# Performance work log

Hardware: AMD Instinct MI355X
Metric: run time of the kernel (lower is better)

Reference implementation:

```python
import jax, jax.numpy as jnp
import numpy as np

BETA = 0.25
B, D, H, W = 32, 256, 32, 32
K = 1024


def setup_inputs() -> dict:
    key = jax.random.key(0)
    k1, k2 = jax.random.split(key)
    inputs = jax.random.normal(k1, (B, D, H, W), dtype=jnp.float32)
    # torch init: uniform(-1/K, 1/K)
    codebook = jax.random.uniform(k2, (K, D), dtype=jnp.float32,
                                  minval=-1.0 / K, maxval=1.0 / K)
    return {"inputs": inputs, "codebook": codebook}


def reference(inputs, codebook):
    b, d, h, w = inputs.shape
    # (B, C, H, W) -> (B*H*W, D)
    x = inputs.transpose(0, 2, 3, 1).reshape(b * h * w, d)
    # Squared Euclidean distances; argmin is identical to cdist argmin.
    x2 = jnp.sum(x * x, axis=1, keepdims=True)            # (N, 1)
    c2 = jnp.sum(codebook * codebook, axis=1)             # (K,)
    d2 = x2 - 2.0 * (x @ codebook.T) + c2[None, :]        # (N, K)
    idx = jnp.argmin(d2, axis=1)                          # (N,)
    q = codebook[idx].reshape(b, h, w, d).transpose(0, 3, 1, 2)  # (B, D, H, W)

    q_loss = jnp.mean((q - jax.lax.stop_gradient(inputs)) ** 2)
    e_loss = jnp.mean((jax.lax.stop_gradient(q) - inputs) ** 2)
    vq_loss = q_loss + BETA * e_loss

    # straight-through estimator
    quantized = inputs + jax.lax.stop_gradient(q - inputs)
    return quantized, q_loss, e_loss, vq_loss, idx.reshape(b, h, w)
```

## Files before the change

kernel.cpp:

```cpp
#include <hip/hip_runtime.h>
#include <cstdint>

typedef float floatx4 __attribute__((ext_vector_type(4)));
typedef _Float16 half8 __attribute__((ext_vector_type(8)));
typedef _Float16 half4v __attribute__((ext_vector_type(4)));

#define D_DIM 256
#define HW 1024
#define K_CODES 1024
#define NPIX 32768
#define NELEM 8388608

#define OFF_QLOSS 8388608
#define OFF_ELOSS 8388609
#define OFF_VQ    8388610
#define OFF_IDX   8388611

#define WS_IDX     0
#define WS_C2      131072
#define WS_CNT     135168
#define WS_PART    135232
#define WS_FLAGPX  143424
#define WS_FLAGTOP 176192
#define WS_CBS     438336
#define FLAG_CAP   8192

#define MARGIN 2.5e-4f

__device__ __forceinline__ float np_pairwise_sq_256(const float* __restrict__ a, int stride) {
    float half[2];
#pragma unroll
    for (int h = 0; h < 2; ++h) {
        const float* p = a + (size_t)(h * 128) * stride;
        float r[8];
#pragma unroll
        for (int j = 0; j < 8; ++j) { float t = p[(size_t)j * stride]; r[j] = __fmul_rn(t, t); }
        for (int i = 8; i < 128; i += 8)
#pragma unroll
            for (int j = 0; j < 8; ++j) {
                float t = p[(size_t)(i + j) * stride];
                r[j] = __fadd_rn(r[j], __fmul_rn(t, t));
            }
        half[h] = __fadd_rn(__fadd_rn(__fadd_rn(r[0], r[1]), __fadd_rn(r[2], r[3])),
                            __fadd_rn(__fadd_rn(r[4], r[5]), __fadd_rn(r[6], r[7])));
    }
    return __fadd_rn(half[0], half[1]);
}

__global__ __launch_bounds__(256) void prep_kernel(const float* __restrict__ cb,
                                                   _Float16* __restrict__ cbs,
                                                   float* __restrict__ c2,
                                                   int* __restrict__ cnt) {
    int b = blockIdx.x;
    if (b < 256) {
        int idx = b * 256 + threadIdx.x;
        int c = idx >> 6;
        int d = (idx & 63) * 4;
        int s = d >> 5, q = (d >> 3) & 3, j0 = d & 7;
        int half = c >> 9, ch = (c >> 4) & 31, l15 = c & 15;
        int lane = q * 16 + l15;
        size_t o = ((((size_t)(half * 32 + ch) * 8 + s) * 64 + lane) * 8 + j0);
        floatx4 v = *(const floatx4*)(cb + (size_t)c * D_DIM + d);
        half4v h;
#pragma unroll
        for (int j = 0; j < 4; ++j) h[j] = (_Float16)(v[j] * 1024.0f);
        *(half4v*)(cbs + o) = h;
    } else {
        if (b == 256 && threadIdx.x == 0) *cnt = 0;
        int k = (b - 256) * 256 + threadIdx.x;
        c2[k] = np_pairwise_sq_256(cb + (size_t)k * D_DIM, 1);
    }
}

__device__ __forceinline__ void ins4v(float v, int k, float* S, int* I) {
    if (v < S[3]) {
        S[3] = v; I[3] = k;
#pragma unroll
        for (int j = 3; j > 0; --j) {
            if (S[j] < S[j - 1]) {
                float ts = S[j]; S[j] = S[j - 1]; S[j - 1] = ts;
                int   ti = I[j]; I[j] = I[j - 1]; I[j - 1] = ti;
            }
        }
    }
}

__global__ __launch_bounds__(256, 2) void gemm_swz(
        const float* __restrict__ x, const _Float16* __restrict__ cbs,
        const float* __restrict__ c2, float* __restrict__ out_idx,
        int* __restrict__ idxbuf, int* __restrict__ cnt,
        int* __restrict__ flagPx, floatx4* __restrict__ flagTop) {
    __shared__ float scr[4][32 * 65];

    const int t = threadIdx.x;
    const int w = t >> 6;
    const int l = t & 63;
    const int l15 = l & 15;
    const int q = l >> 4;
    const int pxg = w >> 1;
    const int half = w & 1;
    const int px0 = blockIdx.x * 64;
    const int bimg = px0 >> 10;
    const int hwb = (px0 & 1023) + pxg * 32;
    const float* xb = x + (size_t)bimg * (D_DIM * HW);

    half8 A[2][8];
#pragma unroll
    for (int r = 0; r < 2; ++r) {
        float tmp[64];
#pragma unroll
        for (int s = 0; s < 8; ++s)
#pragma unroll
            for (int j = 0; j < 8; ++j)
                tmp[s * 8 + j] = xb[(size_t)(s * 32 + q * 8 + j) * HW + hwb + r * 16 + l15];
#pragma unroll
        for (int s = 0; s < 8; ++s) {
            half8 h;
#pragma unroll
            for (int j = 0; j < 8; ++j) h[j] = (_Float16)tmp[s * 8 + j];
            A[r][s] = h;
        }
    }

    const _Float16* base = cbs + (size_t)half * 131072;
    half8 B[2][8];
#pragma unroll
    for (int s = 0; s < 8; ++s)
        B[0][s] = *(const half8*)(base + (size_t)s * 512 + l * 8);
    float c2cur = c2[half * 512 + l15];

    float m1[2][4], m2[2][4]; int i1[2][4], i2[2][4];
#pragma unroll
    for (int r = 0; r < 2; ++r)
#pragma unroll
        for (int a = 0; a < 4; ++a) {
            m1[r][a] = INFINITY; m2[r][a] = INFINITY; i1[r][a] = 0; i2[r][a] = 0;
        }

#pragma unroll 4
    for (int ch = 0; ch < 32; ++ch) {
        const int cur = ch & 1, nxt = cur ^ 1;
        float c2n = 0.f;
        if (ch < 31) {
            const _Float16* nb = base + (size_t)(ch + 1) * 4096;
#pragma unroll
            for (int s = 0; s < 8; ++s)
                B[nxt][s] = *(const half8*)(nb + (size_t)s * 512 + l * 8);
            c2n = c2[half * 512 + (ch + 1) * 16 + l15];
        }
        floatx4 ac[2][2];
#pragma unroll
        for (int r = 0; r < 2; ++r)
#pragma unroll
            for (int h = 0; h < 2; ++h) ac[r][h] = floatx4{0.f, 0.f, 0.f, 0.f};
#pragma unroll
        for (int s = 0; s < 4; ++s) {
            ac[0][0] = __builtin_amdgcn_mfma_f32_16x16x32_f16(A[0][s],     B[cur][s],     ac[0][0], 0, 0, 0);
            ac[1][0] = __builtin_amdgcn_mfma_f32_16x16x32_f16(A[1][s],     B[cur][s],     ac[1][0], 0, 0, 0);
            ac[0][1] = __builtin_amdgcn_mfma_f32_16x16x32_f16(A[0][s + 4], B[cur][s + 4], ac[0][1], 0, 0, 0);
            ac[1][1] = __builtin_amdgcn_mfma_f32_16x16x32_f16(A[1][s + 4], B[cur][s + 4], ac[1][1], 0, 0, 0);
        }
        const int code = half * 512 + ch * 16 + l15;
#pragma unroll
        for (int r = 0; r < 2; ++r)
#pragma unroll
            for (int a = 0; a < 4; ++a) {
                float dot = ac[r][0][a] + ac[r][1][a];
                float s = fmaf(-0.001953125f, dot, c2cur);
                if (s < m1[r][a]) { m2[r][a] = m1[r][a]; i2[r][a] = i1[r][a]; m1[r][a] = s; i1[r][a] = code; }
                else if (s < m2[r][a]) { m2[r][a] = s; i2[r][a] = code; }
            }
        c2cur = c2n;
    }

    const int part = half * 16 + l15;
#pragma unroll
    for (int r = 0; r < 2; ++r)
#pragma unroll
        for (int a = 0; a < 4; ++a) {
            int px = pxg * 32 + r * 16 + q * 4 + a;
            int o = part * 65 + px;
            scr[0][o] = m1[r][a];
            scr[1][o] = __int_as_float(i1[r][a]);
            scr[2][o] = m2[r][a];
            scr[3][o] = __int_as_float(i2[r][a]);
        }
    __syncthreads();
    if (t < 64) {
        float S[4] = {INFINITY, INFINITY, INFINITY, INFINITY};
        int   I[4] = {0x7fffffff, 0x7fffffff, 0x7fffffff, 0x7fffffff};
        for (int p = 0; p < 32; ++p) {
            int o = p * 65 + t;
            ins4v(scr[0][o], __float_as_int(scr[1][o]), S, I);
            ins4v(scr[2][o], __float_as_int(scr[3][o]), S, I);
        }
        int P = px0 + t;
        idxbuf[P] = I[0];
        out_idx[P] = (float)I[0];
        if (S[1] - S[0] <= MARGIN) {
            int pos = atomicAdd(cnt, 1);
            if (pos < FLAG_CAP) {
                flagPx[pos] = P;
                flagTop[2 * pos]     = floatx4{S[0], (float)I[0], S[1], (float)I[1]};
                flagTop[2 * pos + 1] = floatx4{S[2], (float)I[2], S[3], (float)I[3]};
            }
        }
    }
}

__global__ __launch_bounds__(256) void rescore_wave(
        const float* __restrict__ x, const float* __restrict__ cb,
        const float* __restrict__ c2, const int* __restrict__ cnt,
        const int* __restrict__ flagPx, const floatx4* __restrict__ flagTop,
        float* __restrict__ out_idx, int* __restrict__ idxbuf) {
    const int wglobal = blockIdx.x * 4 + (threadIdx.x >> 6);
    const int l = threadIdx.x & 63;
    int n = *cnt; if (n > FLAG_CAP) n = FLAG_CAP;
    for (int i = wglobal; i < n; i += 1024) {
        int P = flagPx[i];
        floatx4 ta = flagTop[2 * i], tb = flagTop[2 * i + 1];
        float s1 = ta[0];
        float cs[4] = {ta[0], ta[2], tb[0], tb[2]};
        int   ck[4] = {(int)ta[1], (int)ta[3], (int)tb[1], (int)tb[3]};
        int nc = 1;
        while (nc < 4 && cs[nc] - s1 <= MARGIN) ++nc;

        const float* xcol = x + (size_t)(P >> 10) * D_DIM * HW + (P & 1023);

        float rj = 0.f;
        if (l < 16) {
            int h = l >> 3, j = l & 7;
            const float* p = xcol + (size_t)(h * 128) * HW;
            float v0 = p[(size_t)j * HW];
            rj = __fmul_rn(v0, v0);
            for (int ii = 1; ii < 16; ++ii) {
                float v = p[(size_t)(ii * 8 + j) * HW];
                rj = __fadd_rn(rj, __fmul_rn(v, v));
            }
        }
        float r0 = __shfl(rj, 0), r1 = __shfl(rj, 1), r2 = __shfl(rj, 2), r3 = __shfl(rj, 3);
        float r4 = __shfl(rj, 4), r5 = __shfl(rj, 5), r6 = __shfl(rj, 6), r7 = __shfl(rj, 7);
        float h0 = __fadd_rn(__fadd_rn(__fadd_rn(r0, r1), __fadd_rn(r2, r3)),
                             __fadd_rn(__fadd_rn(r4, r5), __fadd_rn(r6, r7)));
        r0 = __shfl(rj, 8); r1 = __shfl(rj, 9); r2 = __shfl(rj, 10); r3 = __shfl(rj, 11);
        r4 = __shfl(rj, 12); r5 = __shfl(rj, 13); r6 = __shfl(rj, 14); r7 = __shfl(rj, 15);
        float h1 = __fadd_rn(__fadd_rn(__fadd_rn(r0, r1), __fadd_rn(r2, r3)),
                             __fadd_rn(__fadd_rn(r4, r5), __fadd_rn(r6, r7)));
        float x2 = __fadd_rn(h0, h1);

        float xv[4];
#pragma unroll
        for (int u = 0; u < 4; ++u) xv[u] = xcol[(size_t)(l + u * 64) * HW];
        double accd[4] = {0.0, 0.0, 0.0, 0.0};
        for (int jc = 0; jc < nc; ++jc) {
            const float* cr = cb + (size_t)ck[jc] * D_DIM;
            double a = 0.0;
#pragma unroll
            for (int u = 0; u < 4; ++u) a += (double)xv[u] * (double)cr[l + u * 64];
#pragma unroll
            for (int off = 32; off > 0; off >>= 1) a += __shfl_down(a, off);
            accd[jc] = a;
        }
        if (l == 0) {
            float bd = INFINITY; int bi = 0x7fffffff;
            for (int jc = 0; jc < nc; ++jc) {
                float mm = (float)accd[jc];
                float t1 = __fsub_rn(x2, __fmul_rn(2.0f, mm));
                float Dq = __fadd_rn(t1, c2[ck[jc]]);
                if (Dq < bd || (Dq == bd && ck[jc] < bi)) { bd = Dq; bi = ck[jc]; }
            }
            idxbuf[P] = bi;
            out_idx[P] = (float)bi;
        }
    }
}

__global__ __launch_bounds__(256) void quantize_loss_kernel(
        const float* __restrict__ x, const float* __restrict__ cb,
        const int* __restrict__ idxbuf, float* __restrict__ out_q,
        double* __restrict__ partials) {
    const int t = threadIdx.x;
    const int pxl = t & 31;
    const int dg = t >> 5;
    const int P = blockIdx.x * 32 + pxl;
    const int bimg = P >> 10, hw = P & 1023;
    const float* xb = x + (size_t)bimg * D_DIM * HW + hw;
    float* qb = out_q + (size_t)bimg * D_DIM * HW + hw;
    const floatx4* crow = (const floatx4*)(cb + (size_t)idxbuf[P] * D_DIM) + dg * 8;
    float lsum = 0.f;
#pragma unroll
    for (int i = 0; i < 8; ++i) {
        floatx4 cv = crow[i];
        int dbase = dg * 32 + i * 4;
#pragma unroll
        for (int j = 0; j < 4; ++j) {
            size_t off = (size_t)(dbase + j) * HW;
            float xv = xb[off];
            qb[off] = cv[j];
            float df = cv[j] - xv;
            lsum = fmaf(df, df, lsum);
        }
    }
    double ds = (double)lsum;
#pragma unroll
    for (int off = 32; off > 0; off >>= 1) ds += __shfl_down(ds, off);
    __shared__ double sred[4];
    if ((t & 63) == 0) sred[t >> 6] = ds;
    __syncthreads();
    if (t == 0) partials[blockIdx.x] = sred[0] + sred[1] + sred[2] + sred[3];
}

__global__ __launch_bounds__(64) void finalize_loss(const double* __restrict__ partials,
                                                    float* __restrict__ out) {
    double s = 0.0;
    for (int i = threadIdx.x; i < 1024; i += 64) s += partials[i];
#pragma unroll
    for (int off = 32; off > 0; off >>= 1) s += __shfl_down(s, off);
    if (threadIdx.x == 0) {
        double m = s / (double)NELEM;
        out[OFF_QLOSS] = (float)m;
        out[OFF_ELOSS] = (float)m;
        out[OFF_VQ]    = (float)(1.25 * m);
    }
}

extern "C" void kernel_launch(void* const* d_in, const int* in_sizes, int n_in,
                              void* d_out, int out_size, void* d_ws, size_t ws_size,
                              hipStream_t stream) {
    const float* x  = (const float*)d_in[0];
    const float* cb = (const float*)d_in[1];
    float* out = (float*)d_out;
    char* ws = (char*)d_ws;

    int*      idxbuf  = (int*)(ws + WS_IDX);
    float*    c2      = (float*)(ws + WS_C2);
    int*      cnt     = (int*)(ws + WS_CNT);
    double*   partials= (double*)(ws + WS_PART);
    int*      flagPx  = (int*)(ws + WS_FLAGPX);
    floatx4*  flagTop = (floatx4*)(ws + WS_FLAGTOP);
    _Float16* cbs     = (_Float16*)(ws + WS_CBS);

    prep_kernel<<<260, 256, 0, stream>>>(cb, cbs, c2, cnt);
    gemm_swz<<<NPIX / 64, 256, 0, stream>>>(x, cbs, c2, out + OFF_IDX, idxbuf,
                                            cnt, flagPx, flagTop);
    rescore_wave<<<256, 256, 0, stream>>>(x, cb, c2, cnt, flagPx, flagTop,
                                          out + OFF_IDX, idxbuf);
    quantize_loss_kernel<<<NPIX / 32, 256, 0, stream>>>(x, cb, idxbuf, out, partials);
    finalize_loss<<<1, 64, 0, stream>>>(partials, out);
}
```

Baseline: 152.9 us.

## Fuse quantize and loss into GEMM epilogue, patch rescored pixels with delta loss

The quantize/loss pass is folded into the end of the distance GEMM kernel. Each block gathers its chosen codebook rows, writes the quantized output and sums the squared error right away, so the separate quantize kernel and the index buffer are no longer needed. The rescore kernel now rewrites the output columns only for pixels whose index changed, and adds the loss difference to a double accumulator with an atomic. The B-fragment prefetch is also deepened from one chunk ahead to two, at the cost of more registers, which could hurt occupancy at the two-blocks-per-CU bound.

```diff
diff --git a/kernel.cpp b/kernel.cpp
--- a/kernel.cpp
+++ b/kernel.cpp
@@ -16,13 +16,13 @@
 #define OFF_VQ    8388610
 #define OFF_IDX   8388611
 
-#define WS_IDX     0
-#define WS_C2      131072
-#define WS_CNT     135168
-#define WS_PART    135232
-#define WS_FLAGPX  143424
-#define WS_FLAGTOP 176192
-#define WS_CBS     438336
+#define WS_C2      0
+#define WS_CNT     4096
+#define WS_LFIX    4160
+#define WS_PART    4224
+#define WS_FLAGPX  8320
+#define WS_FLAGTOP 41088
+#define WS_CBS     303232
 #define FLAG_CAP   8192
 
 #define MARGIN 2.5e-4f
@@ -50,7 +50,8 @@
 __global__ __launch_bounds__(256) void prep_kernel(const float* __restrict__ cb,
                                                    _Float16* __restrict__ cbs,
                                                    float* __restrict__ c2,
-                                                   int* __restrict__ cnt) {
+                                                   int* __restrict__ cnt,
+                                                   double* __restrict__ lossFix) {
     int b = blockIdx.x;
     if (b < 256) {
         int idx = b * 256 + threadIdx.x;
@@ -67,6 +68,7 @@
         *(half4v*)(cbs + o) = h;
     } else {
         if (b == 256 && threadIdx.x == 0) *cnt = 0;
+        if (b == 257 && threadIdx.x == 0) *lossFix = 0.0;
         int k = (b - 256) * 256 + threadIdx.x;
         c2[k] = np_pairwise_sq_256(cb + (size_t)k * D_DIM, 1);
     }
@@ -86,11 +88,14 @@
 }
 
 __global__ __launch_bounds__(256, 2) void gemm_swz(
-        const float* __restrict__ x, const _Float16* __restrict__ cbs,
-        const float* __restrict__ c2, float* __restrict__ out_idx,
-        int* __restrict__ idxbuf, int* __restrict__ cnt,
+        const float* __restrict__ x, const float* __restrict__ cb,
+        const _Float16* __restrict__ cbs, const float* __restrict__ c2,
+        float* __restrict__ out_idx, float* __restrict__ out_q,
+        double* __restrict__ partials, int* __restrict__ cnt,
         int* __restrict__ flagPx, floatx4* __restrict__ flagTop) {
     __shared__ float scr[4][32 * 65];
+    __shared__ int sidx[64];
+    __shared__ double sredd[4];
 
     const int t = threadIdx.x;
     const int w = t >> 6;
@@ -123,11 +128,15 @@
     }
 
     const _Float16* base = cbs + (size_t)half * 131072;
-    half8 B[2][8];
-#pragma unroll
-    for (int s = 0; s < 8; ++s)
+    half8 B[4][8];
+#pragma unroll
+    for (int s = 0; s < 8; ++s) {
         B[0][s] = *(const half8*)(base + (size_t)s * 512 + l * 8);
-    float c2cur = c2[half * 512 + l15];
+        B[1][s] = *(const half8*)(base + 4096 + (size_t)s * 512 + l * 8);
+    }
+    float c2b[4];
+    c2b[0] = c2[half * 512 + l15];
+    c2b[1] = c2[half * 512 + 16 + l15];
 
     float m1[2][4], m2[2][4]; int i1[2][4], i2[2][4];
 #pragma unroll
@@ -139,14 +148,14 @@
 
 #pragma unroll 4
     for (int ch = 0; ch < 32; ++ch) {
-        const int cur = ch & 1, nxt = cur ^ 1;
-        float c2n = 0.f;
-        if (ch < 31) {
-            const _Float16* nb = base + (size_t)(ch + 1) * 4096;
+        const int cur = ch & 3;
+        if (ch < 30) {
+            const int pf = (ch + 2) & 3;
+            const _Float16* nb = base + (size_t)(ch + 2) * 4096;
 #pragma unroll
             for (int s = 0; s < 8; ++s)
-                B[nxt][s] = *(const half8*)(nb + (size_t)s * 512 + l * 8);
-            c2n = c2[half * 512 + (ch + 1) * 16 + l15];
+                B[pf][s] = *(const half8*)(nb + (size_t)s * 512 + l * 8);
+            c2b[pf] = c2[half * 512 + (ch + 2) * 16 + l15];
         }
         floatx4 ac[2][2];
 #pragma unroll
@@ -161,6 +170,7 @@
             ac[1][1] = __builtin_amdgcn_mfma_f32_16x16x32_f16(A[1][s + 4], B[cur][s + 4], ac[1][1], 0, 0, 0);
         }
         const int code = half * 512 + ch * 16 + l15;
+        const float c2cur = c2b[cur];
 #pragma unroll
         for (int r = 0; r < 2; ++r)
 #pragma unroll
@@ -170,7 +180,6 @@
                 if (s < m1[r][a]) { m2[r][a] = m1[r][a]; i2[r][a] = i1[r][a]; m1[r][a] = s; i1[r][a] = code; }
                 else if (s < m2[r][a]) { m2[r][a] = s; i2[r][a] = code; }
             }
-        c2cur = c2n;
     }
 
     const int part = half * 16 + l15;
@@ -195,7 +204,7 @@
             ins4v(scr[2][o], __float_as_int(scr[3][o]), S, I);
         }
         int P = px0 + t;
-        idxbuf[P] = I[0];
+        sidx[t] = I[0];
         out_idx[P] = (float)I[0];
         if (S[1] - S[0] <= MARGIN) {
             int pos = atomicAdd(cnt, 1);
@@ -206,13 +215,45 @@
             }
         }
     }
-}
-
-__global__ __launch_bounds__(256) void rescore_wave(
+    __syncthreads();
+
+    {
+        const int dq = t >> 6;
+        const int pxl = t & 63;
+        const int myidx = sidx[pxl];
+        const int hwofs = (px0 & 1023) + pxl;
+        const float* xcol = x + (size_t)bimg * (D_DIM * HW) + hwofs;
+        float* qcol = out_q + (size_t)bimg * (D_DIM * HW) + hwofs;
+        const floatx4* crow = (const floatx4*)(cb + (size_t)myidx * D_DIM) + dq * 16;
+        float lsum = 0.f;
+#pragma unroll
+        for (int i = 0; i < 16; ++i) {
+            floatx4 cv = crow[i];
+            int dbase = dq * 64 + i * 4;
+#pragma unroll
+            for (int j = 0; j < 4; ++j) {
+                size_t off = (size_t)(dbase + j) * HW;
+                float xv = xcol[off];
+                qcol[off] = cv[j];
+                float df = cv[j] - xv;
+                lsum = fmaf(df, df, lsum);
+            }
+        }
+        double ds = (double)lsum;
+#pragma unroll
+        for (int off = 32; off > 0; off >>= 1) ds += __shfl_down(ds, off);
+        if (l == 0) sredd[w] = ds;
+    }
+    __syncthreads();
+    if (t == 0) partials[blockIdx.x] = sredd[0] + sredd[1] + sredd[2] + sredd[3];
+}
+
+__global__ __launch_bounds__(256) void rescore_fix(
         const float* __restrict__ x, const float* __restrict__ cb,
         const float* __restrict__ c2, const int* __restrict__ cnt,
         const int* __restrict__ flagPx, const floatx4* __restrict__ flagTop,
-        float* __restrict__ out_idx, int* __restrict__ idxbuf) {
+        float* __restrict__ out_idx, float* __restrict__ out_q,
+        double* __restrict__ lossFix) {
     const int wglobal = blockIdx.x * 4 + (threadIdx.x >> 6);
     const int l = threadIdx.x & 63;
     int n = *cnt; if (n > FLAG_CAP) n = FLAG_CAP;
@@ -225,7 +266,8 @@
         int nc = 1;
         while (nc < 4 && cs[nc] - s1 <= MARGIN) ++nc;
 
-        const float* xcol = x + (size_t)(P >> 10) * D_DIM * HW + (P & 1023);
+        const size_t colbase = (size_t)(P >> 10) * (D_DIM * HW) + (P & 1023);
+        const float* xcol = x + colbase;
 
         float rj = 0.f;
         if (l < 16) {
@@ -258,66 +300,48 @@
 #pragma unroll
             for (int u = 0; u < 4; ++u) a += (double)xv[u] * (double)cr[l + u * 64];
 #pragma unroll
-            for (int off = 32; off > 0; off >>= 1) a += __shfl_down(a, off);
+            for (int off = 32; off > 0; off >>= 1) a += __shfl_xor(a, off);
             accd[jc] = a;
         }
-        if (l == 0) {
-            float bd = INFINITY; int bi = 0x7fffffff;
-            for (int jc = 0; jc < nc; ++jc) {
-                float mm = (float)accd[jc];
-                float t1 = __fsub_rn(x2, __fmul_rn(2.0f, mm));
-                float Dq = __fadd_rn(t1, c2[ck[jc]]);
-                if (Dq < bd || (Dq == bd && ck[jc] < bi)) { bd = Dq; bi = ck[jc]; }
-            }
-            idxbuf[P] = bi;
-            out_idx[P] = (float)bi;
-        }
-    }
-}
-
-__global__ __launch_bounds__(256) void quantize_loss_kernel(
-        const float* __restrict__ x, const float* __restrict__ cb,
-        const int* __restrict__ idxbuf, float* __restrict__ out_q,
-        double* __restrict__ partials) {
-    const int t = threadIdx.x;
-    const int pxl = t & 31;
-    const int dg = t >> 5;
-    const int P = blockIdx.x * 32 + pxl;
-    const int bimg = P >> 10, hw = P & 1023;
-    const float* xb = x + (size_t)bimg * D_DIM * HW + hw;
-    float* qb = out_q + (size_t)bimg * D_DIM * HW + hw;
-    const floatx4* crow = (const floatx4*)(cb + (size_t)idxbuf[P] * D_DIM) + dg * 8;
-    float lsum = 0.f;
-#pragma unroll
-    for (int i = 0; i < 8; ++i) {
-        floatx4 cv = crow[i];
-        int dbase = dg * 32 + i * 4;
-#pragma unroll
-        for (int j = 0; j < 4; ++j) {
-            size_t off = (size_t)(dbase + j) * HW;
-            float xv = xb[off];
-            qb[off] = cv[j];
-            float df = cv[j] - xv;
-            lsum = fmaf(df, df, lsum);
-        }
-    }
-    double ds = (double)lsum;
-#pragma unroll
-    for (int off = 32; off > 0; off >>= 1) ds += __shfl_down(ds, off);
-    __shared__ double sred[4];
-    if ((t & 63) == 0) sred[t >> 6] = ds;
-    __syncthreads();
-    if (t == 0) partials[blockIdx.x] = sred[0] + sred[1] + sred[2] + sred[3];
+        float bd = INFINITY; int bi = 0x7fffffff;
+        for (int jc = 0; jc < nc; ++jc) {
+            float mm = (float)accd[jc];
+            float t1 = __fsub_rn(x2, __fmul_rn(2.0f, mm));
+            float Dq = __fadd_rn(t1, c2[ck[jc]]);
+            if (Dq < bd || (Dq == bd && ck[jc] < bi)) { bd = Dq; bi = ck[jc]; }
+        }
+        int oldI = (int)ta[1];
+        if (l == 0) out_idx[P] = (float)bi;
+        if (bi != oldI) {
+            const float* cn = cb + (size_t)bi * D_DIM;
+            const float* co = cb + (size_t)oldI * D_DIM;
+            float* qcol = out_q + colbase;
+            double dd = 0.0;
+#pragma unroll
+            for (int u = 0; u < 4; ++u) {
+                int d = l + u * 64;
+                float cnd = cn[d], cod = co[d];
+                double dn = (double)cnd - (double)xv[u];
+                double do_ = (double)cod - (double)xv[u];
+                dd += dn * dn - do_ * do_;
+                qcol[(size_t)d * HW] = cnd;
+            }
+#pragma unroll
+            for (int off = 32; off > 0; off >>= 1) dd += __shfl_xor(dd, off);
+            if (l == 0) atomicAdd(lossFix, dd);
+        }
+    }
 }
 
 __global__ __launch_bounds__(64) void finalize_loss(const double* __restrict__ partials,
+                                                    const double* __restrict__ lossFix,
                                                     float* __restrict__ out) {
     double s = 0.0;
-    for (int i = threadIdx.x; i < 1024; i += 64) s += partials[i];
+    for (int i = threadIdx.x; i < 512; i += 64) s += partials[i];
 #pragma unroll
     for (int off = 32; off > 0; off >>= 1) s += __shfl_down(s, off);
     if (threadIdx.x == 0) {
-        double m = s / (double)NELEM;
+        double m = (s + *lossFix) / (double)NELEM;
         out[OFF_QLOSS] = (float)m;
         out[OFF_ELOSS] = (float)m;
         out[OFF_VQ]    = (float)(1.25 * m);
@@ -332,19 +356,18 @@
     float* out = (float*)d_out;
     char* ws = (char*)d_ws;
 
-    int*      idxbuf  = (int*)(ws + WS_IDX);
     float*    c2      = (float*)(ws + WS_C2);
     int*      cnt     = (int*)(ws + WS_CNT);
+    double*   lossFix = (double*)(ws + WS_LFIX);
     double*   partials= (double*)(ws + WS_PART);
     int*      flagPx  = (int*)(ws + WS_FLAGPX);
     floatx4*  flagTop = (floatx4*)(ws + WS_FLAGTOP);
     _Float16* cbs     = (_Float16*)(ws + WS_CBS);
 
-    prep_kernel<<<260, 256, 0, stream>>>(cb, cbs, c2, cnt);
-    gemm_swz<<<NPIX / 64, 256, 0, stream>>>(x, cbs, c2, out + OFF_IDX, idxbuf,
-                                            cnt, flagPx, flagTop);
-    rescore_wave<<<256, 256, 0, stream>>>(x, cb, c2, cnt, flagPx, flagTop,
-                                          out + OFF_IDX, idxbuf);
-    quantize_loss_kernel<<<NPIX / 32, 256, 0, stream>>>(x, cb, idxbuf, out, partials);
-    finalize_loss<<<1, 64, 0, stream>>>(partials, out);
-}
+    prep_kernel<<<260, 256, 0, stream>>>(cb, cbs, c2, cnt, lossFix);
+    gemm_swz<<<NPIX / 64, 256, 0, stream>>>(x, cb, cbs, c2, out + OFF_IDX, out,
+                                            partials, cnt, flagPx, flagTop);
+    rescore_fix<<<256, 256, 0, stream>>>(x, cb, c2, cnt, flagPx, flagTop,
+                                         out + OFF_IDX, out, lossFix);
+    finalize_loss<<<1, 64, 0, stream>>>(partials, lossFix, out);
+}
```

Result: slower. 170.3 us (+11.4%).

## Fuse rescore, quantize and loss finalize into one kernel with packed top-4

Applied to the files above, without the earlier changes.

The separate rescore, quantize-loss and finalize kernels are merged into one kernel, reducing five launches to three. The GEMM now writes a packed top-4 per pixel (truncated score bits plus a 10-bit code index), and each block rescores its own ambiguous pixels locally, dropping the global atomic flag list. A last-block-done counter computes the final loss reduction. The c2+1 offset keeps scores positive so the bit-packing preserves ordering. Truncating the scores loses precision, so the margin was widened, which means more pixels get rescored.

```diff
diff --git a/kernel.cpp b/kernel.cpp
--- a/kernel.cpp
+++ b/kernel.cpp
@@ -16,16 +16,14 @@
 #define OFF_VQ    8388610
 #define OFF_IDX   8388611
 
-#define WS_IDX     0
-#define WS_C2      131072
-#define WS_CNT     135168
-#define WS_PART    135232
-#define WS_FLAGPX  143424
-#define WS_FLAGTOP 176192
-#define WS_CBS     438336
-#define FLAG_CAP   8192
-
-#define MARGIN 2.5e-4f
+#define WS_C2      0
+#define WS_C2P     4096
+#define WS_DONE    8192
+#define WS_PART    8256
+#define WS_PK4     16448
+#define WS_CBS     540736
+
+#define MARGIN 5.0e-4f
 
 __device__ __forceinline__ float np_pairwise_sq_256(const float* __restrict__ a, int stride) {
     float half[2];
@@ -50,7 +48,8 @@
 __global__ __launch_bounds__(256) void prep_kernel(const float* __restrict__ cb,
                                                    _Float16* __restrict__ cbs,
                                                    float* __restrict__ c2,
-                                                   int* __restrict__ cnt) {
+                                                   float* __restrict__ c2p,
+                                                   int* __restrict__ done) {
     int b = blockIdx.x;
     if (b < 256) {
         int idx = b * 256 + threadIdx.x;
@@ -66,9 +65,11 @@
         for (int j = 0; j < 4; ++j) h[j] = (_Float16)(v[j] * 1024.0f);
         *(half4v*)(cbs + o) = h;
     } else {
-        if (b == 256 && threadIdx.x == 0) *cnt = 0;
+        if (b == 256 && threadIdx.x == 0) *done = 0;
         int k = (b - 256) * 256 + threadIdx.x;
-        c2[k] = np_pairwise_sq_256(cb + (size_t)k * D_DIM, 1);
+        float v = np_pairwise_sq_256(cb + (size_t)k * D_DIM, 1);
+        c2[k] = v;
+        c2p[k] = __fadd_rn(v, 1.0f);
     }
 }
 
@@ -87,9 +88,7 @@
 
 __global__ __launch_bounds__(256, 2) void gemm_swz(
         const float* __restrict__ x, const _Float16* __restrict__ cbs,
-        const float* __restrict__ c2, float* __restrict__ out_idx,
-        int* __restrict__ idxbuf, int* __restrict__ cnt,
-        int* __restrict__ flagPx, floatx4* __restrict__ flagTop) {
+        const float* __restrict__ c2p, uint4* __restrict__ pk4) {
     __shared__ float scr[4][32 * 65];
 
     const int t = threadIdx.x;
@@ -127,7 +126,7 @@
 #pragma unroll
     for (int s = 0; s < 8; ++s)
         B[0][s] = *(const half8*)(base + (size_t)s * 512 + l * 8);
-    float c2cur = c2[half * 512 + l15];
+    float c2cur = c2p[half * 512 + l15];
 
     float m1[2][4], m2[2][4]; int i1[2][4], i2[2][4];
 #pragma unroll
@@ -146,7 +145,7 @@
 #pragma unroll
             for (int s = 0; s < 8; ++s)
                 B[nxt][s] = *(const half8*)(nb + (size_t)s * 512 + l * 8);
-            c2n = c2[half * 512 + (ch + 1) * 16 + l15];
+            c2n = c2p[half * 512 + (ch + 1) * 16 + l15];
         }
         floatx4 ac[2][2];
 #pragma unroll
@@ -194,38 +193,62 @@
             ins4v(scr[0][o], __float_as_int(scr[1][o]), S, I);
             ins4v(scr[2][o], __float_as_int(scr[3][o]), S, I);
         }
-        int P = px0 + t;
-        idxbuf[P] = I[0];
-        out_idx[P] = (float)I[0];
-        if (S[1] - S[0] <= MARGIN) {
-            int pos = atomicAdd(cnt, 1);
-            if (pos < FLAG_CAP) {
-                flagPx[pos] = P;
-                flagTop[2 * pos]     = floatx4{S[0], (float)I[0], S[1], (float)I[1]};
-                flagTop[2 * pos + 1] = floatx4{S[2], (float)I[2], S[3], (float)I[3]};
-            }
-        }
-    }
-}
-
-__global__ __launch_bounds__(256) void rescore_wave(
+        uint4 pk;
+        pk.x = (__float_as_uint(S[0]) & 0xFFFFFC00u) | (unsigned)I[0];
+        pk.y = (__float_as_uint(S[1]) & 0xFFFFFC00u) | (unsigned)I[1];
+        pk.z = (__float_as_uint(S[2]) & 0xFFFFFC00u) | (unsigned)I[2];
+        pk.w = (__float_as_uint(S[3]) & 0xFFFFFC00u) | (unsigned)I[3];
+        pk4[px0 + t] = pk;
+    }
+}
+
+__global__ __launch_bounds__(256) void quant_rescore(
         const float* __restrict__ x, const float* __restrict__ cb,
-        const float* __restrict__ c2, const int* __restrict__ cnt,
-        const int* __restrict__ flagPx, const floatx4* __restrict__ flagTop,
-        float* __restrict__ out_idx, int* __restrict__ idxbuf) {
-    const int wglobal = blockIdx.x * 4 + (threadIdx.x >> 6);
-    const int l = threadIdx.x & 63;
-    int n = *cnt; if (n > FLAG_CAP) n = FLAG_CAP;
-    for (int i = wglobal; i < n; i += 1024) {
-        int P = flagPx[i];
-        floatx4 ta = flagTop[2 * i], tb = flagTop[2 * i + 1];
-        float s1 = ta[0];
-        float cs[4] = {ta[0], ta[2], tb[0], tb[2]};
-        int   ck[4] = {(int)ta[1], (int)ta[3], (int)tb[1], (int)tb[3]};
+        const float* __restrict__ c2, const uint4* __restrict__ pk4,
+        float* __restrict__ out_idx, float* __restrict__ out_q,
+        double* __restrict__ partials, int* __restrict__ done,
+        float* __restrict__ out) {
+    __shared__ int sFinal[32];
+    __shared__ int sCand[32][4];
+    __shared__ int sNc[32];
+    __shared__ int sList[32];
+    __shared__ int sNum;
+    __shared__ double sred[4];
+    __shared__ bool amLast;
+
+    const int t = threadIdx.x;
+    const int px0 = blockIdx.x * 32;
+    const int bimg = px0 >> 10;
+    const float* xbase = x + (size_t)bimg * (D_DIM * HW);
+
+    if (t == 0) sNum = 0;
+    __syncthreads();
+
+    if (t < 32) {
+        uint4 pk = pk4[px0 + t];
+        unsigned pu[4] = {pk.x, pk.y, pk.z, pk.w};
+        float S0 = __uint_as_float(pu[0] & 0xFFFFFC00u);
         int nc = 1;
-        while (nc < 4 && cs[nc] - s1 <= MARGIN) ++nc;
-
-        const float* xcol = x + (size_t)(P >> 10) * D_DIM * HW + (P & 1023);
+#pragma unroll
+        for (int j = 1; j < 4; ++j) {
+            float Sj = __uint_as_float(pu[j] & 0xFFFFFC00u);
+            if (nc == j && Sj - S0 <= MARGIN) ++nc;
+        }
+        sFinal[t] = (int)(pu[0] & 1023u);
+#pragma unroll
+        for (int j = 0; j < 4; ++j) sCand[t][j] = (int)(pu[j] & 1023u);
+        sNc[t] = nc;
+        if (nc > 1) { int pos = atomicAdd(&sNum, 1); sList[pos] = t; }
+    }
+    __syncthreads();
+
+    const int w = t >> 6, l = t & 63;
+    const int nflag = sNum;
+    for (int fi = w; fi < nflag; fi += 4) {
+        const int pxl = sList[fi];
+        const int nc = sNc[pxl];
+        const int hw = (px0 & 1023) + pxl;
+        const float* xcol = xbase + hw;
 
         float rj = 0.f;
         if (l < 16) {
@@ -251,76 +274,72 @@
         float xv[4];
 #pragma unroll
         for (int u = 0; u < 4; ++u) xv[u] = xcol[(size_t)(l + u * 64) * HW];
-        double accd[4] = {0.0, 0.0, 0.0, 0.0};
+        float bd = INFINITY; int bi = 0x7fffffff;
         for (int jc = 0; jc < nc; ++jc) {
-            const float* cr = cb + (size_t)ck[jc] * D_DIM;
+            int ckj = sCand[pxl][jc];
+            const float* cr = cb + (size_t)ckj * D_DIM;
             double a = 0.0;
 #pragma unroll
             for (int u = 0; u < 4; ++u) a += (double)xv[u] * (double)cr[l + u * 64];
 #pragma unroll
-            for (int off = 32; off > 0; off >>= 1) a += __shfl_down(a, off);
-            accd[jc] = a;
-        }
-        if (l == 0) {
-            float bd = INFINITY; int bi = 0x7fffffff;
-            for (int jc = 0; jc < nc; ++jc) {
-                float mm = (float)accd[jc];
-                float t1 = __fsub_rn(x2, __fmul_rn(2.0f, mm));
-                float Dq = __fadd_rn(t1, c2[ck[jc]]);
-                if (Dq < bd || (Dq == bd && ck[jc] < bi)) { bd = Dq; bi = ck[jc]; }
-            }
-            idxbuf[P] = bi;
-            out_idx[P] = (float)bi;
-        }
-    }
-}
-
-__global__ __launch_bounds__(256) void quantize_loss_kernel(
-        const float* __restrict__ x, const float* __restrict__ cb,
-        const int* __restrict__ idxbuf, float* __restrict__ out_q,
-        double* __restrict__ partials) {
-    const int t = threadIdx.x;
-    const int pxl = t & 31;
-    const int dg = t >> 5;
-    const int P = blockIdx.x * 32 + pxl;
-    const int bimg = P >> 10, hw = P & 1023;
-    const float* xb = x + (size_t)bimg * D_DIM * HW + hw;
-    float* qb = out_q + (size_t)bimg * D_DIM * HW + hw;
-    const floatx4* crow = (const floatx4*)(cb + (size_t)idxbuf[P] * D_DIM) + dg * 8;
-    float lsum = 0.f;
-#pragma unroll
-    for (int i = 0; i < 8; ++i) {
-        floatx4 cv = crow[i];
-        int dbase = dg * 32 + i * 4;
-#pragma unroll
-        for (int j = 0; j < 4; ++j) {
-            size_t off = (size_t)(dbase + j) * HW;
-            float xv = xb[off];
-            qb[off] = cv[j];
-            float df = cv[j] - xv;
-            lsum = fmaf(df, df, lsum);
-        }
-    }
-    double ds = (double)lsum;
-#pragma unroll
-    for (int off = 32; off > 0; off >>= 1) ds += __shfl_down(ds, off);
-    __shared__ double sred[4];
-    if ((t & 63) == 0) sred[t >> 6] = ds;
+            for (int off = 32; off > 0; off >>= 1) a += __shfl_xor(a, off);
+            float mm = (float)a;
+            float t1 = __fsub_rn(x2, __fmul_rn(2.0f, mm));
+            float Dq = __fadd_rn(t1, c2[ckj]);
+            if (Dq < bd || (Dq == bd && ckj < bi)) { bd = Dq; bi = ckj; }
+        }
+        if (l == 0) sFinal[pxl] = bi;
+    }
+    __syncthreads();
+
+    {
+        const int pxl = t & 31;
+        const int dg = t >> 5;
+        const int P = px0 + pxl;
+        const int hw = P & 1023;
+        const int myidx = sFinal[pxl];
+        if (t < 32) out_idx[P] = (float)myidx;
+        const float* xcol = xbase + hw;
+        float* qcol = out_q + (size_t)bimg * (D_DIM * HW) + hw;
+        const floatx4* crow = (const floatx4*)(cb + (size_t)myidx * D_DIM) + dg * 8;
+        float lsum = 0.f;
+#pragma unroll
+        for (int i = 0; i < 8; ++i) {
+            floatx4 cv = crow[i];
+            int dbase = dg * 32 + i * 4;
+#pragma unroll
+            for (int j = 0; j < 4; ++j) {
+                size_t off = (size_t)(dbase + j) * HW;
+                float xvv = xcol[off];
+                qcol[off] = cv[j];
+                float df = cv[j] - xvv;
+                lsum = fmaf(df, df, lsum);
+            }
+        }
+        double ds = (double)lsum;
+#pragma unroll
+        for (int off = 32; off > 0; off >>= 1) ds += __shfl_down(ds, off);
+        if ((t & 63) == 0) sred[t >> 6] = ds;
+    }
     __syncthreads();
     if (t == 0) partials[blockIdx.x] = sred[0] + sred[1] + sred[2] + sred[3];
-}
-
-__global__ __launch_bounds__(64) void finalize_loss(const double* __restrict__ partials,
-                                                    float* __restrict__ out) {
-    double s = 0.0;
-    for (int i = threadIdx.x; i < 1024; i += 64) s += partials[i];
-#pragma unroll
-    for (int off = 32; off > 0; off >>= 1) s += __shfl_down(s, off);
-    if (threadIdx.x == 0) {
-        double m = s / (double)NELEM;
-        out[OFF_QLOSS] = (float)m;
-        out[OFF_ELOSS] = (float)m;
-        out[OFF_VQ]    = (float)(1.25 * m);
+
+    __threadfence();
+    if (t == 0) amLast = (atomicAdd(done, 1) == (int)gridDim.x - 1);
+    __syncthreads();
+    if (amLast) {
+        double s = 0.0;
+        for (int i = t; i < 1024; i += 256) s += partials[i];
+#pragma unroll
+        for (int off = 32; off > 0; off >>= 1) s += __shfl_down(s, off);
+        if ((t & 63) == 0) sred[t >> 6] = s;
+        __syncthreads();
+        if (t == 0) {
+            double m = (sred[0] + sred[1] + sred[2] + sred[3]) / (double)NELEM;
+            out[OFF_QLOSS] = (float)m;
+            out[OFF_ELOSS] = (float)m;
+            out[OFF_VQ]    = (float)(1.25 * m);
+        }
     }
 }
 
@@ -332,19 +351,15 @@
     float* out = (float*)d_out;
     char* ws = (char*)d_ws;
 
-    int*      idxbuf  = (int*)(ws + WS_IDX);
     float*    c2      = (float*)(ws + WS_C2);
-    int*      cnt     = (int*)(ws + WS_CNT);
+    float*    c2p     = (float*)(ws + WS_C2P);
+    int*      done    = (int*)(ws + WS_DONE);
     double*   partials= (double*)(ws + WS_PART);
-    int*      flagPx  = (int*)(ws + WS_FLAGPX);
-    floatx4*  flagTop = (floatx4*)(ws + WS_FLAGTOP);
+    uint4*    pk4     = (uint4*)(ws + WS_PK4);
     _Float16* cbs     = (_Float16*)(ws + WS_CBS);
 
-    prep_kernel<<<260, 256, 0, stream>>>(cb, cbs, c2, cnt);
-    gemm_swz<<<NPIX / 64, 256, 0, stream>>>(x, cbs, c2, out + OFF_IDX, idxbuf,
-                                            cnt, flagPx, flagTop);
-    rescore_wave<<<256, 256, 0, stream>>>(x, cb, c2, cnt, flagPx, flagTop,
-                                          out + OFF_IDX, idxbuf);
-    quantize_loss_kernel<<<NPIX / 32, 256, 0, stream>>>(x, cb, idxbuf, out, partials);
-    finalize_loss<<<1, 64, 0, stream>>>(partials, out);
-}
+    prep_kernel<<<260, 256, 0, stream>>>(cb, cbs, c2, c2p, done);
+    gemm_swz<<<NPIX / 64, 256, 0, stream>>>(x, cbs, c2p, pk4);
+    quant_rescore<<<NPIX / 32, 256, 0, stream>>>(x, cb, c2, pk4, out + OFF_IDX,
+                                                 out, partials, done, out);
+}
```

New measurement: 301.3 us. 1.97x slower.
